# Kernel optimization log

Measured on AMD Instinct MI355X. Metric: run time of the kernel, lower is better.

The kernel has to match this reference:

```python
import jax, jax.numpy as jnp
import numpy as np

B, T, M, P = 512, 64, 256, 256


def setup_inputs() -> dict:
    key = jax.random.key(0)
    ks = jax.random.split(key, 17)
    w = lambda i, shape: (jax.random.normal(ks[i], shape, jnp.float32) * 0.05)
    return {
        "encoded_inputs": jax.random.normal(ks[0], (B, T, M), jnp.float32),
        "y": jax.random.normal(ks[1], (B, T, 1), jnp.float32),
        "tar": jax.random.normal(ks[2], (B, 2), jnp.float32),
        "train": 1,
        "Wd_w": w(3, (M, 2 * P)), "Wd_b": w(4, (M,)),
        "Ud_w": w(5, (M, M)),
        "vd_w": w(6, (1, M)),
        "wt_w": w(7, (1, M + 1)), "wt_b": w(8, (1,)),
        "Wy_w": w(9, (P, P + M)), "Wy_b": w(10, (P,)),
        "vy_w": w(11, (1, P)), "vy_b": w(12, (1,)),
        "Wih": w(13, (4 * P, 1)), "Whh": w(14, (4 * P, P)),
        "bih": w(15, (4 * P,)), "bhh": w(16, (4 * P,)),
    }


def _lstm_cell(x, h, c, Wih, Whh, bih, bhh):
    # torch.nn.LSTMCell gate order: i, f, g, o
    g = x @ Wih.T + h @ Whh.T + (bih + bhh)
    i, f, gg, o = jnp.split(g, 4, axis=1)
    c = jax.nn.sigmoid(f) * c + jax.nn.sigmoid(i) * jnp.tanh(gg)
    h = jax.nn.sigmoid(o) * jnp.tanh(c)
    return h, c


def reference(encoded_inputs, y, tar, train,
              Wd_w, Wd_b, Ud_w, vd_w, wt_w, wt_b,
              Wy_w, Wy_b, vy_w, vy_b, Wih, Whh, bih, bhh):
    Bn = encoded_inputs.shape[0]
    Pn = Whh.shape[1]
    Mn = encoded_inputs.shape[2]
    h0 = jnp.zeros((Bn, Pn), encoded_inputs.dtype)
    c0 = jnp.zeros((Bn, Pn), encoded_inputs.dtype)
    ctx0 = jnp.zeros((Bn, Mn), encoded_inputs.dtype)
    # U_d(encoded_inputs) is loop-invariant
    y1 = jnp.einsum('btm,nm->btn', encoded_inputs, Ud_w)  # (B,T,M)

    def attend(h, s):
        x1 = jnp.concatenate([h, s], axis=1) @ Wd_w.T + Wd_b      # (B,M)
        z1 = jnp.tanh(x1[:, None, :] + y1)                        # (B,T,M)
        l = jnp.einsum('btm,m->bt', z1, vd_w[0])                  # (B,T)
        beta = jax.nn.softmax(l, axis=1)
        return jnp.einsum('bt,btm->bm', beta, encoded_inputs)     # (B,M)

    def step(carry, y_t):
        h, s, _ = carry
        c_t = attend(h, s)
        y_til = jnp.concatenate([c_t, y_t], axis=1) @ wt_w.T + wt_b  # (B,1)
        h, s = _lstm_cell(y_til, h, s, Wih, Whh, bih, bhh)
        return (h, s, c_t), None

    (h, s, c_t), _ = jax.lax.scan(step, (h0, c0, ctx0), jnp.swapaxes(y, 0, 1))

    def head(h):
        return (jnp.concatenate([h, c_t], axis=1) @ Wy_w.T + Wy_b) @ vy_w.T + vy_b

    def extra(h, s, inp):
        y_til = jnp.concatenate([c_t, inp], axis=1) @ wt_w.T + wt_b
        h, s = _lstm_cell(y_til, h, s, Wih, Whh, bih, bhh)
        return h, s, head(h)

    y_Tp1 = head(h)
    if train:
        h, s, y_Tp2 = extra(h, s, tar[:, 0:1])
        h, s, y_Tp3 = extra(h, s, tar[:, 1:2])
    else:
        h, s, y_Tp2 = extra(h, s, y_Tp1)
        h, s, y_Tp3 = extra(h, s, y_Tp2)
    return (y_Tp1, y_Tp2, y_Tp3)
```

## Files before the change

kernel.cpp:

```cpp
#include <hip/hip_runtime.h>


typedef unsigned short u16;
typedef unsigned int u32;
typedef _Float16 half_t;
typedef half_t h2 __attribute__((ext_vector_type(2)));

#define BB 512
#define TT 64
#define MM 256
#define PP 256
#define YS 264

#define WD16_OFF  0
#define WHH16_OFF 131072
#define WY16_OFF  393216
#define WQ_ELEMS  524288
#define E16_OFF   524288
#define E16_ELEMS (BB * TT * MM)
#define WS_ELEMS  (WQ_ELEMS + E16_ELEMS)
#define WS_BYTES  (WS_ELEMS * 2)

struct H8 { h2 p[4]; };

#if defined(__has_builtin)
#if __has_builtin(__builtin_amdgcn_fdot2)
#define FDOT2(a, b, c) __builtin_amdgcn_fdot2((a), (b), (c), false)
#endif
#endif
#ifndef FDOT2
__device__ __forceinline__ float FDOT2(h2 a, h2 b, float c) {
  return c + (float)a[0] * (float)b[0] + (float)a[1] * (float)b[1];
}
#endif

__device__ __forceinline__ float dot8(const H8 w, const H8 a, float acc) {
  acc = FDOT2(w.p[0], a.p[0], acc);
  acc = FDOT2(w.p[1], a.p[1], acc);
  acc = FDOT2(w.p[2], a.p[2], acc);
  acc = FDOT2(w.p[3], a.p[3], acc);
  return acc;
}
__device__ __forceinline__ u16 f2h(float f) {
  union { half_t h; u16 u; } x; x.h = (half_t)f; return x.u;
}
__device__ __forceinline__ void unpackH8(const H8 v, float f[8]) {
#pragma unroll
  for (int i = 0; i < 8; ++i) f[i] = (float)v.p[i >> 1][i & 1];
}
__device__ __forceinline__ void ldf8(const float* p, float f[8]) {
  float4 a = *(const float4*)p;
  float4 b = *(const float4*)(p + 4);
  f[0]=a.x; f[1]=a.y; f[2]=a.z; f[3]=a.w;
  f[4]=b.x; f[5]=b.y; f[6]=b.z; f[7]=b.w;
}
__device__ __forceinline__ float tanh_fast(float x) {
  float e = __builtin_amdgcn_exp2f(x * 2.885390081777927f);
  return 1.0f - 2.0f * __builtin_amdgcn_rcpf(1.0f + e);
}
__device__ __forceinline__ float sigmoid_fast(float x) {
  float e = __builtin_amdgcn_exp2f(x * -1.4426950408889634f);
  return __builtin_amdgcn_rcpf(1.0f + e);
}

__global__ __launch_bounds__(256) void prep_w(
    const float* __restrict__ Wd, const float* __restrict__ Whh,
    const float* __restrict__ Wy, u16* __restrict__ o) {
  int i = blockIdx.x * 256 + threadIdx.x;
  float v;
  if (i < WHH16_OFF) {
    int ki = i & 7, n = (i >> 3) & 255, kb = i >> 11;
    v = Wd[n * 512 + kb * 8 + ki];
  } else if (i < WY16_OFF) {
    int r = i - WHH16_OFF;
    int ki = r & 7, n = (r >> 3) & 1023, kb = r >> 13;
    v = Whh[n * 256 + kb * 8 + ki];
  } else {
    int r = i - WY16_OFF;
    int ki = r & 7, n = (r >> 3) & 255, kb = r >> 11;
    v = Wy[n * 512 + kb * 8 + ki];
  }
  o[i] = f2h(v);
}

__global__ __launch_bounds__(256) void prep_e(
    const float* __restrict__ E, u16* __restrict__ o) {
  int i = blockIdx.x * 256 + threadIdx.x;
  o[E16_OFF + i] = f2h(E[i]);
}

template <int WQ>
__global__ __launch_bounds__(512, 2) void scan_kernel(
    const float* __restrict__ E,
    const float* __restrict__ yin,
    const float* __restrict__ tar,
    const int*   __restrict__ train,
    const void*  __restrict__ Wd_q,
    const float* __restrict__ Wd_b,
    const float* __restrict__ Ud_w,
    const float* __restrict__ vd_w,
    const float* __restrict__ wt_w,
    const float* __restrict__ wt_b,
    const void*  __restrict__ Wy_q,
    const float* __restrict__ Wy_b,
    const float* __restrict__ vy_w,
    const float* __restrict__ vy_b,
    const float* __restrict__ Wih,
    const void*  __restrict__ Whh_q,
    const float* __restrict__ bih,
    const float* __restrict__ bhh,
    const u16*   __restrict__ E16,
    float* __restrict__ out)
{
  __shared__ __align__(16) u16   y1l[2][TT * YS];
  __shared__ __align__(16) u32   hs16[2 * 256];
  __shared__ __align__(16) u32   ctx16p[2 * 128];
  __shared__ __align__(16) float gbuf[2][1024];
  __shared__ __align__(16) float part[2][2][256];
  __shared__ __align__(16) float x1s[2][MM];
  __shared__ __align__(16) float ctx[2][MM];
  __shared__ __align__(16) float lpart[2][4][TT];
  __shared__ float red[2][4];
  __shared__ float sc_head[2];

  const int tid  = threadIdx.x;
  const int half = tid >> 8;
  const int j    = tid & 255;
  const int wv   = (tid >> 6) & 3;
  const int lane = tid & 63;
  const int b    = blockIdx.x * 2 + half;

  hs16[tid] = 0;
  float creg = 0.f;

  {
    const float* __restrict__ Eb = E + (size_t)b * TT * MM;
    const float* __restrict__ Uj = Ud_w + (size_t)j * MM;
    for (int t0 = 0; t0 < TT; t0 += 16) {
      float acc[16];
#pragma unroll
      for (int i = 0; i < 16; ++i) acc[i] = 0.f;
      for (int m0 = 0; m0 < MM; m0 += 8) {
        float w[8]; ldf8(Uj + m0, w);
#pragma unroll
        for (int tt = 0; tt < 16; ++tt) {
          float e[8]; ldf8(Eb + (size_t)(t0 + tt) * MM + m0, e);
#pragma unroll
          for (int mm = 0; mm < 8; ++mm) acc[tt] = fmaf(e[mm], w[mm], acc[tt]);
        }
      }
#pragma unroll
      for (int tt = 0; tt < 16; ++tt)
        y1l[half][(t0 + tt) * YS + j] = f2h(acc[tt]);
    }
  }
  __syncthreads();

  auto whh_mv = [&]() {
    float b00 = 0.f, b01 = 0.f, b10 = 0.f, b11 = 0.f;
    if (WQ) {
      const u16* p1 = (const u16*)Whh_q + (size_t)tid * 8;
      const u16* p2 = p1 + 512 * 8;
#pragma unroll 4
      for (int kb = 0; kb < 32; ++kb) {
        H8 h0 = *(const H8*)&hs16[kb * 4];
        H8 h1 = *(const H8*)&hs16[256 + kb * 4];
        H8 w1 = *(const H8*)p1; p1 += 8192;
        H8 w2 = *(const H8*)p2; p2 += 8192;
        b00 = dot8(w1, h0, b00);
        b01 = dot8(w1, h1, b01);
        b10 = dot8(w2, h0, b10);
        b11 = dot8(w2, h1, b11);
      }
    } else {
      const float* q1 = (const float*)Whh_q + (size_t)tid * 256;
      const float* q2 = q1 + 512 * 256;
#pragma unroll 2
      for (int kb = 0; kb < 32; ++kb) {
        H8 h0 = *(const H8*)&hs16[kb * 4];
        H8 h1 = *(const H8*)&hs16[256 + kb * 4];
        float f0[8], f1[8]; unpackH8(h0, f0); unpackH8(h1, f1);
        float w1[8], w2[8];
        ldf8(q1 + kb * 8, w1);
        ldf8(q2 + kb * 8, w2);
#pragma unroll
        for (int i = 0; i < 8; ++i) {
          b00 = fmaf(f0[i], w1[i], b00);
          b01 = fmaf(f1[i], w1[i], b01);
          b10 = fmaf(f0[i], w2[i], b10);
          b11 = fmaf(f1[i], w2[i], b11);
        }
      }
    }
    gbuf[0][tid] = b00;       gbuf[1][tid] = b01;
    gbuf[0][tid + 512] = b10; gbuf[1][tid + 512] = b11;
  };

  auto gates_apply = [&](float ytil) {
    float g0 = gbuf[half][j]       + ytil * Wih[j]       + bih[j]       + bhh[j];
    float g1 = gbuf[half][j + 256] + ytil * Wih[j + 256] + bih[j + 256] + bhh[j + 256];
    float g2 = gbuf[half][j + 512] + ytil * Wih[j + 512] + bih[j + 512] + bhh[j + 512];
    float g3 = gbuf[half][j + 768] + ytil * Wih[j + 768] + bih[j + 768] + bhh[j + 768];
    float c = sigmoid_fast(g1) * creg + sigmoid_fast(g0) * tanh_fast(g2);
    float h = sigmoid_fast(g3) * tanh_fast(c);
    creg = c;
    u16* hsu = (u16*)hs16;
    hsu[half * 512 + j]       = f2h(h);
    hsu[half * 512 + 256 + j] = f2h(c);
  };

  auto head_store = [&](int outIdx) {
    float p0 = 0.f, p1 = 0.f;
    if (WQ) {
      const u16* pw = (const u16*)Wy_q + (size_t)half * 32 * 2048 + (size_t)j * 8;
      const u32* a0 = half ? &ctx16p[0] : &hs16[0];
      const u32* a1 = half ? &ctx16p[128] : &hs16[256];
#pragma unroll 4
      for (int kb = 0; kb < 32; ++kb) {
        H8 w = *(const H8*)pw; pw += 2048;
        p0 = dot8(w, *(const H8*)&a0[kb * 4], p0);
        p1 = dot8(w, *(const H8*)&a1[kb * 4], p1);
      }
    } else {
      const float* pw = (const float*)Wy_q + (size_t)j * 512 + half * 256;
      for (int kb = 0; kb < 32; ++kb) {
        float w[8]; ldf8(pw + kb * 8, w);
        if (half) {
#pragma unroll
          for (int i = 0; i < 8; ++i) {
            p0 = fmaf(ctx[0][kb * 8 + i], w[i], p0);
            p1 = fmaf(ctx[1][kb * 8 + i], w[i], p1);
          }
        } else {
          H8 h0 = *(const H8*)&hs16[kb * 4];
          H8 h1 = *(const H8*)&hs16[256 + kb * 4];
          float f0[8], f1[8]; unpackH8(h0, f0); unpackH8(h1, f1);
#pragma unroll
          for (int i = 0; i < 8; ++i) {
            p0 = fmaf(f0[i], w[i], p0);
            p1 = fmaf(f1[i], w[i], p1);
          }
        }
      }
    }
    part[half][0][j] = p0;
    part[half][1][j] = p1;
    __syncthreads();
    {
      float hp = part[0][half][j] + part[1][half][j] + Wy_b[j];
      float pp = hp * vy_w[j];
#pragma unroll
      for (int off = 32; off; off >>= 1) pp += __shfl_xor(pp, off, 64);
      if (lane == 0) red[half][wv] = pp;
    }
    __syncthreads();
    if (j == 0) {
      float o = red[half][0] + red[half][1] + red[half][2] + red[half][3]
              + vy_b[0];
      out[(size_t)outIdx * BB + b] = o;
      sc_head[half] = o;
    }
    __syncthreads();
  };

  for (int step = 0; step < TT; ++step) {
    {
      float ax0 = 0.f, ax1 = 0.f;
      float b00 = 0.f, b01 = 0.f, b10 = 0.f, b11 = 0.f;
      if (WQ) {
        const u16* pd = (const u16*)Wd_q + (size_t)half * 32 * 2048 + (size_t)j * 8;
        const u16* p1 = (const u16*)Whh_q + (size_t)tid * 8;
        const u16* p2 = p1 + 512 * 8;
        const int ao = half * 128;
#pragma unroll 4
        for (int kb = 0; kb < 32; ++kb) {
          H8 h0 = *(const H8*)&hs16[kb * 4];
          H8 h1 = *(const H8*)&hs16[256 + kb * 4];
          H8 a0 = *(const H8*)&hs16[ao + kb * 4];
          H8 a1 = *(const H8*)&hs16[256 + ao + kb * 4];
          H8 wd = *(const H8*)pd; pd += 2048;
          H8 w1 = *(const H8*)p1; p1 += 8192;
          H8 w2 = *(const H8*)p2; p2 += 8192;
          ax0 = dot8(wd, a0, ax0);
          ax1 = dot8(wd, a1, ax1);
          b00 = dot8(w1, h0, b00);
          b01 = dot8(w1, h1, b01);
          b10 = dot8(w2, h0, b10);
          b11 = dot8(w2, h1, b11);
        }
      } else {
        const float* pd = (const float*)Wd_q + (size_t)j * 512 + half * 256;
        const float* q1 = (const float*)Whh_q + (size_t)tid * 256;
        const float* q2 = q1 + 512 * 256;
        const int ao = half * 128;
#pragma unroll 2
        for (int kb = 0; kb < 32; ++kb) {
          H8 h0 = *(const H8*)&hs16[kb * 4];
          H8 h1 = *(const H8*)&hs16[256 + kb * 4];
          H8 c0 = *(const H8*)&hs16[ao + kb * 4];
          H8 c1 = *(const H8*)&hs16[256 + ao + kb * 4];
          float f0[8], f1[8], e0[8], e1[8];
          unpackH8(h0, f0); unpackH8(h1, f1); unpackH8(c0, e0); unpackH8(c1, e1);
          float wd[8], w1[8], w2[8];
          ldf8(pd + kb * 8, wd);
          ldf8(q1 + kb * 8, w1);
          ldf8(q2 + kb * 8, w2);
#pragma unroll
          for (int i = 0; i < 8; ++i) {
            ax0 = fmaf(e0[i], wd[i], ax0);
            ax1 = fmaf(e1[i], wd[i], ax1);
            b00 = fmaf(f0[i], w1[i], b00);
            b01 = fmaf(f1[i], w1[i], b01);
            b10 = fmaf(f0[i], w2[i], b10);
            b11 = fmaf(f1[i], w2[i], b11);
          }
        }
      }
      part[half][0][j] = ax0;
      part[half][1][j] = ax1;
      gbuf[0][tid] = b00;       gbuf[1][tid] = b01;
      gbuf[0][tid + 512] = b10; gbuf[1][tid + 512] = b11;
    }
    __syncthreads();
    x1s[half][j] = part[0][half][j] + part[1][half][j] + Wd_b[j];
    __syncthreads();

    {
      const u16* __restrict__ yrow = &y1l[half][lane * YS + wv * 64];
      const float* __restrict__ xp = &x1s[half][wv * 64];
      const float* __restrict__ vp = vd_w + wv * 64;
      float lp = 0.f;
#pragma unroll 2
      for (int m0 = 0; m0 < 64; m0 += 8) {
        H8 yv = *(const H8*)(yrow + m0);
        float yf[8]; unpackH8(yv, yf);
        float xf[8]; ldf8(xp + m0, xf);
        float vf[8]; ldf8(vp + m0, vf);
#pragma unroll
        for (int mm = 0; mm < 8; ++mm) {
          float z = tanh_fast(xf[mm] + yf[mm]);
          lp = fmaf(z, vf[mm], lp);
        }
      }
      lpart[half][wv][lane] = lp;
    }
    __syncthreads();

    float ctv;
    {
      float l = lpart[half][0][lane] + lpart[half][1][lane]
              + lpart[half][2][lane] + lpart[half][3][lane];
      float mx = l;
#pragma unroll
      for (int off = 32; off; off >>= 1) mx = fmaxf(mx, __shfl_xor(mx, off, 64));
      float e = __builtin_amdgcn_exp2f((l - mx) * 1.4426950408889634f);
      float sm = e;
#pragma unroll
      for (int off = 32; off; off >>= 1) sm += __shfl_xor(sm, off, 64);
      float beta = e * __builtin_amdgcn_rcpf(sm);

      float acc = 0.f;
      if (WQ) {
        const half_t* __restrict__ ep = (const half_t*)E16 + (size_t)b * TT * MM + j;
#pragma unroll 8
        for (int t = 0; t < TT; ++t) {
          float bt = __shfl(beta, t, 64);
          acc = fmaf(bt, (float)ep[(size_t)t * MM], acc);
        }
      } else {
        const float* __restrict__ ep = E + (size_t)b * TT * MM + j;
#pragma unroll 8
        for (int t = 0; t < TT; ++t) {
          float bt = __shfl(beta, t, 64);
          acc = fmaf(bt, ep[(size_t)t * MM], acc);
        }
      }
      ctv = acc;
      ctx[half][j] = acc;
      ((u16*)ctx16p)[half * 256 + j] = f2h(acc);

      float p = ctv * wt_w[j];
#pragma unroll
      for (int off = 32; off; off >>= 1) p += __shfl_xor(p, off, 64);
      if (lane == 0) red[half][wv] = p;
    }
    __syncthreads();

    {
      float ytil = red[half][0] + red[half][1] + red[half][2] + red[half][3]
                 + yin[(size_t)b * TT + step] * wt_w[MM] + wt_b[0];
      gates_apply(ytil);
    }
    __syncthreads();
  }

  float ctdot;
  {
    float p = ctx[half][j] * wt_w[j];
#pragma unroll
    for (int off = 32; off; off >>= 1) p += __shfl_xor(p, off, 64);
    if (lane == 0) red[half][wv] = p;
    __syncthreads();
    ctdot = red[half][0] + red[half][1] + red[half][2] + red[half][3];
  }

  head_store(0);

  const int tr = train[0];
  for (int e = 0; e < 2; ++e) {
    float inp = tr ? tar[(size_t)b * 2 + e] : sc_head[half];
    float ytil = ctdot + inp * wt_w[MM] + wt_b[0];
    whh_mv();
    __syncthreads();
    gates_apply(ytil);
    __syncthreads();
    head_store(1 + e);
  }
}

extern "C" void kernel_launch(void* const* d_in, const int* in_sizes, int n_in,
                              void* d_out, int out_size, void* d_ws, size_t ws_size,
                              hipStream_t stream) {
  const float* E     = (const float*)d_in[0];
  const float* yin   = (const float*)d_in[1];
  const float* tar   = (const float*)d_in[2];
  const int*   train = (const int*)d_in[3];
  const float* Wd_w  = (const float*)d_in[4];
  const float* Wd_b  = (const float*)d_in[5];
  const float* Ud_w  = (const float*)d_in[6];
  const float* vd_w  = (const float*)d_in[7];
  const float* wt_w  = (const float*)d_in[8];
  const float* wt_b  = (const float*)d_in[9];
  const float* Wy_w  = (const float*)d_in[10];
  const float* Wy_b  = (const float*)d_in[11];
  const float* vy_w  = (const float*)d_in[12];
  const float* vy_b  = (const float*)d_in[13];
  const float* Wih   = (const float*)d_in[14];
  const float* Whh   = (const float*)d_in[15];
  const float* bih   = (const float*)d_in[16];
  const float* bhh   = (const float*)d_in[17];

  float* out = (float*)d_out;

  if (ws_size >= (size_t)WS_BYTES) {
    u16* wq = (u16*)d_ws;
    prep_w<<<dim3(WQ_ELEMS / 256), dim3(256), 0, stream>>>(Wd_w, Whh, Wy_w, wq);
    prep_e<<<dim3(E16_ELEMS / 256), dim3(256), 0, stream>>>(E, wq);
    scan_kernel<1><<<dim3(BB / 2), dim3(512), 0, stream>>>(
        E, yin, tar, train, wq + WD16_OFF, Wd_b, Ud_w, vd_w, wt_w, wt_b,
        wq + WY16_OFF, Wy_b, vy_w, vy_b, Wih, wq + WHH16_OFF, bih, bhh,
        wq + E16_OFF, out);
  } else {
    scan_kernel<0><<<dim3(BB / 2), dim3(512), 0, stream>>>(
        E, yin, tar, train, Wd_w, Wd_b, Ud_w, vd_w, wt_w, wt_b,
        Wy_w, Wy_b, vy_w, vy_b, Wih, Whh, bih, bhh, (const u16*)nullptr, out);
  }

  (void)in_sizes; (void)n_in; (void)out_size;
}
```

Measured before the change: 1.195 ms.

## Double block to 1024 threads, split matvecs along K, and use fp16 Ud projection

The scan kernel now runs 1024 threads per block, still covering two batch rows. The Wd, Wy and context reductions are split across four or two K-partitions with shared-memory partial sums, and each Whh gate row gets its own thread. The Ud_w projection is precomputed into an fp16 packed layout and computed with fdot2 from the fp16 E copy. This exposes more parallelism per recurrent step in exchange for extra barriers and partial-sum traffic, and possibly lower occupancy because of the 1024-thread launch bound and register pressure.

```diff
diff --git a/kernel.cpp b/kernel.cpp
--- a/kernel.cpp
+++ b/kernel.cpp
@@ -15,11 +15,12 @@
 #define WD16_OFF  0
 #define WHH16_OFF 131072
 #define WY16_OFF  393216
-#define WQ_ELEMS  524288
-#define E16_OFF   524288
+#define UD16_OFF  524288
+#define WPREP_ELEMS 589824
+#define E16_OFF   589824
 #define E16_ELEMS (BB * TT * MM)
-#define WS_ELEMS  (WQ_ELEMS + E16_ELEMS)
-#define WS_BYTES  (WS_ELEMS * 2)
+#define WS_ELEMS  (WPREP_ELEMS + E16_ELEMS)
+#define WS_BYTES  ((size_t)WS_ELEMS * 2)
 
 struct H8 { h2 p[4]; };
 
@@ -65,7 +66,8 @@
 
 __global__ __launch_bounds__(256) void prep_w(
     const float* __restrict__ Wd, const float* __restrict__ Whh,
-    const float* __restrict__ Wy, u16* __restrict__ o) {
+    const float* __restrict__ Wy, const float* __restrict__ Ud,
+    u16* __restrict__ o) {
   int i = blockIdx.x * 256 + threadIdx.x;
   float v;
   if (i < WHH16_OFF) {
@@ -75,10 +77,14 @@
     int r = i - WHH16_OFF;
     int ki = r & 7, n = (r >> 3) & 1023, kb = r >> 13;
     v = Whh[n * 256 + kb * 8 + ki];
-  } else {
+  } else if (i < UD16_OFF) {
     int r = i - WY16_OFF;
     int ki = r & 7, n = (r >> 3) & 255, kb = r >> 11;
     v = Wy[n * 512 + kb * 8 + ki];
+  } else {
+    int r = i - UD16_OFF;
+    int ki = r & 7, n = (r >> 3) & 255, kb = r >> 11;
+    v = Ud[n * 256 + kb * 8 + ki];
   }
   o[i] = f2h(v);
 }
@@ -90,14 +96,14 @@
 }
 
 template <int WQ>
-__global__ __launch_bounds__(512, 2) void scan_kernel(
+__global__ __launch_bounds__(1024, 4) void scan_kernel(
     const float* __restrict__ E,
     const float* __restrict__ yin,
     const float* __restrict__ tar,
     const int*   __restrict__ train,
     const void*  __restrict__ Wd_q,
     const float* __restrict__ Wd_b,
-    const float* __restrict__ Ud_w,
+    const void*  __restrict__ Ud_q,
     const float* __restrict__ vd_w,
     const float* __restrict__ wt_w,
     const float* __restrict__ wt_b,
@@ -113,152 +119,157 @@
     float* __restrict__ out)
 {
   __shared__ __align__(16) u16   y1l[2][TT * YS];
-  __shared__ __align__(16) u32   hs16[2 * 256];
-  __shared__ __align__(16) u32   ctx16p[2 * 128];
+  __shared__ __align__(16) u32   hs16[2][256];
+  __shared__ __align__(16) u32   ctx16p[2][128];
+  __shared__ __align__(16) float ctx[2][256];
+  __shared__ __align__(16) float x1s[2][256];
+  __shared__ __align__(16) float part[4][2][256];
+  __shared__ __align__(16) float part2[2][2][256];
   __shared__ __align__(16) float gbuf[2][1024];
-  __shared__ __align__(16) float part[2][2][256];
-  __shared__ __align__(16) float x1s[2][MM];
-  __shared__ __align__(16) float ctx[2][MM];
-  __shared__ __align__(16) float lpart[2][4][TT];
-  __shared__ float red[2][4];
+  __shared__ __align__(16) float lpart[2][8][64];
+  __shared__ float red[2][4], red2[2][4];
   __shared__ float sc_head[2];
 
   const int tid  = threadIdx.x;
-  const int half = tid >> 8;
-  const int j    = tid & 255;
-  const int wv   = (tid >> 6) & 3;
   const int lane = tid & 63;
-  const int b    = blockIdx.x * 2 + half;
-
-  hs16[tid] = 0;
+  const int w    = tid >> 6;
+  const int n    = tid & 255;
+  const int kq   = tid >> 8;
+  const int rw   = w >> 2;
+  const int jj   = (w & 3) * 64 + lane;
+  const int r1   = w >> 3;
+  const int mq   = w & 7;
+  const int kh   = (w >> 2) & 1;
+  const int j2   = (w & 3) * 64 + lane;
+
+  if (tid < 512) ((u32*)hs16)[tid] = 0;
   float creg = 0.f;
 
   {
-    const float* __restrict__ Eb = E + (size_t)b * TT * MM;
-    const float* __restrict__ Uj = Ud_w + (size_t)j * MM;
-    for (int t0 = 0; t0 < TT; t0 += 16) {
-      float acc[16];
-#pragma unroll
-      for (int i = 0; i < 16; ++i) acc[i] = 0.f;
-      for (int m0 = 0; m0 < MM; m0 += 8) {
-        float w[8]; ldf8(Uj + m0, w);
-#pragma unroll
-        for (int tt = 0; tt < 16; ++tt) {
-          float e[8]; ldf8(Eb + (size_t)(t0 + tt) * MM + m0, e);
-#pragma unroll
-          for (int mm = 0; mm < 8; ++mm) acc[tt] = fmaf(e[mm], w[mm], acc[tt]);
-        }
-      }
-#pragma unroll
-      for (int tt = 0; tt < 16; ++tt)
-        y1l[half][(t0 + tt) * YS + j] = f2h(acc[tt]);
+    const int yr  = kq >> 1;
+    const int th  = kq & 1;
+    const int bb  = blockIdx.x * 2 + yr;
+    if (WQ) {
+      const half_t* __restrict__ Ef = (const half_t*)E16;
+      for (int t = th * 32; t < th * 32 + 32; ++t) {
+        const half_t* ee = Ef + ((size_t)bb * TT + t) * MM;
+        const u16* pu = (const u16*)Ud_q + (size_t)n * 8;
+        float acc = 0.f;
+#pragma unroll 8
+        for (int kb = 0; kb < 32; ++kb) {
+          H8 uw = *(const H8*)pu; pu += 2048;
+          H8 ev = *(const H8*)(ee + kb * 8);
+          acc = dot8(uw, ev, acc);
+        }
+        y1l[yr][t * YS + n] = f2h(acc);
+      }
+    } else {
+      const float* __restrict__ Eb = E + (size_t)bb * TT * MM;
+      const float* __restrict__ Uj = (const float*)Ud_q + (size_t)n * MM;
+      for (int t = th * 32; t < th * 32 + 32; ++t) {
+        float acc = 0.f;
+        for (int m0 = 0; m0 < MM; m0 += 8) {
+          float uu[8], ee[8];
+          ldf8(Uj + m0, uu);
+          ldf8(Eb + (size_t)t * MM + m0, ee);
+#pragma unroll
+          for (int i = 0; i < 8; ++i) acc = fmaf(uu[i], ee[i], acc);
+        }
+        y1l[yr][t * YS + n] = f2h(acc);
+      }
     }
   }
   __syncthreads();
 
   auto whh_mv = [&]() {
-    float b00 = 0.f, b01 = 0.f, b10 = 0.f, b11 = 0.f;
+    float b0 = 0.f, b1 = 0.f;
     if (WQ) {
-      const u16* p1 = (const u16*)Whh_q + (size_t)tid * 8;
-      const u16* p2 = p1 + 512 * 8;
+      const u16* ph = (const u16*)Whh_q + (size_t)tid * 8;
+#pragma unroll 8
+      for (int kb = 0; kb < 32; ++kb) {
+        H8 w8 = *(const H8*)ph; ph += 8192;
+        b0 = dot8(w8, *(const H8*)&hs16[0][kb * 4], b0);
+        b1 = dot8(w8, *(const H8*)&hs16[1][kb * 4], b1);
+      }
+    } else {
+      const float* ph = (const float*)Whh_q + (size_t)tid * 256;
 #pragma unroll 4
       for (int kb = 0; kb < 32; ++kb) {
-        H8 h0 = *(const H8*)&hs16[kb * 4];
-        H8 h1 = *(const H8*)&hs16[256 + kb * 4];
-        H8 w1 = *(const H8*)p1; p1 += 8192;
-        H8 w2 = *(const H8*)p2; p2 += 8192;
-        b00 = dot8(w1, h0, b00);
-        b01 = dot8(w1, h1, b01);
-        b10 = dot8(w2, h0, b10);
-        b11 = dot8(w2, h1, b11);
-      }
-    } else {
-      const float* q1 = (const float*)Whh_q + (size_t)tid * 256;
-      const float* q2 = q1 + 512 * 256;
-#pragma unroll 2
-      for (int kb = 0; kb < 32; ++kb) {
-        H8 h0 = *(const H8*)&hs16[kb * 4];
-        H8 h1 = *(const H8*)&hs16[256 + kb * 4];
-        float f0[8], f1[8]; unpackH8(h0, f0); unpackH8(h1, f1);
-        float w1[8], w2[8];
-        ldf8(q1 + kb * 8, w1);
-        ldf8(q2 + kb * 8, w2);
+        float w8[8]; ldf8(ph + kb * 8, w8);
+        float f0[8], f1[8];
+        unpackH8(*(const H8*)&hs16[0][kb * 4], f0);
+        unpackH8(*(const H8*)&hs16[1][kb * 4], f1);
 #pragma unroll
         for (int i = 0; i < 8; ++i) {
-          b00 = fmaf(f0[i], w1[i], b00);
-          b01 = fmaf(f1[i], w1[i], b01);
-          b10 = fmaf(f0[i], w2[i], b10);
-          b11 = fmaf(f1[i], w2[i], b11);
-        }
-      }
-    }
-    gbuf[0][tid] = b00;       gbuf[1][tid] = b01;
-    gbuf[0][tid + 512] = b10; gbuf[1][tid + 512] = b11;
+          b0 = fmaf(f0[i], w8[i], b0);
+          b1 = fmaf(f1[i], w8[i], b1);
+        }
+      }
+    }
+    gbuf[0][tid] = b0;
+    gbuf[1][tid] = b1;
   };
 
   auto gates_apply = [&](float ytil) {
-    float g0 = gbuf[half][j]       + ytil * Wih[j]       + bih[j]       + bhh[j];
-    float g1 = gbuf[half][j + 256] + ytil * Wih[j + 256] + bih[j + 256] + bhh[j + 256];
-    float g2 = gbuf[half][j + 512] + ytil * Wih[j + 512] + bih[j + 512] + bhh[j + 512];
-    float g3 = gbuf[half][j + 768] + ytil * Wih[j + 768] + bih[j + 768] + bhh[j + 768];
+    float g0 = gbuf[rw][jj]       + ytil * Wih[jj]       + bih[jj]       + bhh[jj];
+    float g1 = gbuf[rw][jj + 256] + ytil * Wih[jj + 256] + bih[jj + 256] + bhh[jj + 256];
+    float g2 = gbuf[rw][jj + 512] + ytil * Wih[jj + 512] + bih[jj + 512] + bhh[jj + 512];
+    float g3 = gbuf[rw][jj + 768] + ytil * Wih[jj + 768] + bih[jj + 768] + bhh[jj + 768];
     float c = sigmoid_fast(g1) * creg + sigmoid_fast(g0) * tanh_fast(g2);
     float h = sigmoid_fast(g3) * tanh_fast(c);
     creg = c;
-    u16* hsu = (u16*)hs16;
-    hsu[half * 512 + j]       = f2h(h);
-    hsu[half * 512 + 256 + j] = f2h(c);
+    ((u16*)&hs16[rw][0])[jj]       = f2h(h);
+    ((u16*)&hs16[rw][0])[256 + jj] = f2h(c);
   };
 
   auto head_store = [&](int outIdx) {
     float p0 = 0.f, p1 = 0.f;
     if (WQ) {
-      const u16* pw = (const u16*)Wy_q + (size_t)half * 32 * 2048 + (size_t)j * 8;
-      const u32* a0 = half ? &ctx16p[0] : &hs16[0];
-      const u32* a1 = half ? &ctx16p[128] : &hs16[256];
-#pragma unroll 4
-      for (int kb = 0; kb < 32; ++kb) {
-        H8 w = *(const H8*)pw; pw += 2048;
-        p0 = dot8(w, *(const H8*)&a0[kb * 4], p0);
-        p1 = dot8(w, *(const H8*)&a1[kb * 4], p1);
+      const u16* pw = (const u16*)Wy_q + ((size_t)(kq * 16) * 256 + n) * 8;
+      const u32* a0 = (kq < 2) ? &hs16[0][kq * 64] : &ctx16p[0][(kq - 2) * 64];
+      const u32* a1 = (kq < 2) ? &hs16[1][kq * 64] : &ctx16p[1][(kq - 2) * 64];
+#pragma unroll 8
+      for (int i = 0; i < 16; ++i) {
+        H8 w8 = *(const H8*)pw; pw += 2048;
+        p0 = dot8(w8, *(const H8*)&a0[i * 4], p0);
+        p1 = dot8(w8, *(const H8*)&a1[i * 4], p1);
       }
     } else {
-      const float* pw = (const float*)Wy_q + (size_t)j * 512 + half * 256;
-      for (int kb = 0; kb < 32; ++kb) {
-        float w[8]; ldf8(pw + kb * 8, w);
-        if (half) {
-#pragma unroll
-          for (int i = 0; i < 8; ++i) {
-            p0 = fmaf(ctx[0][kb * 8 + i], w[i], p0);
-            p1 = fmaf(ctx[1][kb * 8 + i], w[i], p1);
-          }
+      const float* pw = (const float*)Wy_q + (size_t)n * 512 + kq * 128;
+      for (int i = 0; i < 16; ++i) {
+        float w8[8]; ldf8(pw + i * 8, w8);
+        int kb = kq * 16 + i;
+        float f0[8], f1[8];
+        if (kb < 32) {
+          unpackH8(*(const H8*)&hs16[0][kb * 4], f0);
+          unpackH8(*(const H8*)&hs16[1][kb * 4], f1);
         } else {
-          H8 h0 = *(const H8*)&hs16[kb * 4];
-          H8 h1 = *(const H8*)&hs16[256 + kb * 4];
-          float f0[8], f1[8]; unpackH8(h0, f0); unpackH8(h1, f1);
-#pragma unroll
-          for (int i = 0; i < 8; ++i) {
-            p0 = fmaf(f0[i], w[i], p0);
-            p1 = fmaf(f1[i], w[i], p1);
-          }
-        }
-      }
-    }
-    part[half][0][j] = p0;
-    part[half][1][j] = p1;
-    __syncthreads();
-    {
-      float hp = part[0][half][j] + part[1][half][j] + Wy_b[j];
-      float pp = hp * vy_w[j];
+          ldf8(&ctx[0][(kb - 32) * 8], f0);
+          ldf8(&ctx[1][(kb - 32) * 8], f1);
+        }
+#pragma unroll
+        for (int i2 = 0; i2 < 8; ++i2) {
+          p0 = fmaf(f0[i2], w8[i2], p0);
+          p1 = fmaf(f1[i2], w8[i2], p1);
+        }
+      }
+    }
+    part[kq][0][n] = p0;
+    part[kq][1][n] = p1;
+    __syncthreads();
+    if (w < 8) {
+      float hp = part[0][rw][jj] + part[1][rw][jj] + part[2][rw][jj]
+               + part[3][rw][jj] + Wy_b[jj];
+      float pp = hp * vy_w[jj];
 #pragma unroll
       for (int off = 32; off; off >>= 1) pp += __shfl_xor(pp, off, 64);
-      if (lane == 0) red[half][wv] = pp;
-    }
-    __syncthreads();
-    if (j == 0) {
-      float o = red[half][0] + red[half][1] + red[half][2] + red[half][3]
-              + vy_b[0];
-      out[(size_t)outIdx * BB + b] = o;
-      sc_head[half] = o;
+      if (lane == 0) red[rw][w & 3] = pp;
+    }
+    __syncthreads();
+    if (w < 8 && (w & 3) == 0 && lane == 0) {
+      float o = red[rw][0] + red[rw][1] + red[rw][2] + red[rw][3] + vy_b[0];
+      out[(size_t)outIdx * BB + blockIdx.x * 2 + rw] = o;
+      sc_head[rw] = o;
     }
     __syncthreads();
   };
@@ -266,72 +277,51 @@
   for (int step = 0; step < TT; ++step) {
     {
       float ax0 = 0.f, ax1 = 0.f;
-      float b00 = 0.f, b01 = 0.f, b10 = 0.f, b11 = 0.f;
       if (WQ) {
-        const u16* pd = (const u16*)Wd_q + (size_t)half * 32 * 2048 + (size_t)j * 8;
-        const u16* p1 = (const u16*)Whh_q + (size_t)tid * 8;
-        const u16* p2 = p1 + 512 * 8;
-        const int ao = half * 128;
-#pragma unroll 4
-        for (int kb = 0; kb < 32; ++kb) {
-          H8 h0 = *(const H8*)&hs16[kb * 4];
-          H8 h1 = *(const H8*)&hs16[256 + kb * 4];
-          H8 a0 = *(const H8*)&hs16[ao + kb * 4];
-          H8 a1 = *(const H8*)&hs16[256 + ao + kb * 4];
-          H8 wd = *(const H8*)pd; pd += 2048;
-          H8 w1 = *(const H8*)p1; p1 += 8192;
-          H8 w2 = *(const H8*)p2; p2 += 8192;
-          ax0 = dot8(wd, a0, ax0);
-          ax1 = dot8(wd, a1, ax1);
-          b00 = dot8(w1, h0, b00);
-          b01 = dot8(w1, h1, b01);
-          b10 = dot8(w2, h0, b10);
-          b11 = dot8(w2, h1, b11);
+        const u16* pd = (const u16*)Wd_q + ((size_t)(kq * 16) * 256 + n) * 8;
+        const u32* a0 = (kq < 2) ? &hs16[0][kq * 64] : &hs16[0][128 + (kq - 2) * 64];
+        const u32* a1 = (kq < 2) ? &hs16[1][kq * 64] : &hs16[1][128 + (kq - 2) * 64];
+#pragma unroll 8
+        for (int i = 0; i < 16; ++i) {
+          H8 w8 = *(const H8*)pd; pd += 2048;
+          ax0 = dot8(w8, *(const H8*)&a0[i * 4], ax0);
+          ax1 = dot8(w8, *(const H8*)&a1[i * 4], ax1);
         }
       } else {
-        const float* pd = (const float*)Wd_q + (size_t)j * 512 + half * 256;
-        const float* q1 = (const float*)Whh_q + (size_t)tid * 256;
-        const float* q2 = q1 + 512 * 256;
-        const int ao = half * 128;
-#pragma unroll 2
-        for (int kb = 0; kb < 32; ++kb) {
-          H8 h0 = *(const H8*)&hs16[kb * 4];
-          H8 h1 = *(const H8*)&hs16[256 + kb * 4];
-          H8 c0 = *(const H8*)&hs16[ao + kb * 4];
-          H8 c1 = *(const H8*)&hs16[256 + ao + kb * 4];
-          float f0[8], f1[8], e0[8], e1[8];
-          unpackH8(h0, f0); unpackH8(h1, f1); unpackH8(c0, e0); unpackH8(c1, e1);
-          float wd[8], w1[8], w2[8];
-          ldf8(pd + kb * 8, wd);
-          ldf8(q1 + kb * 8, w1);
-          ldf8(q2 + kb * 8, w2);
-#pragma unroll
-          for (int i = 0; i < 8; ++i) {
-            ax0 = fmaf(e0[i], wd[i], ax0);
-            ax1 = fmaf(e1[i], wd[i], ax1);
-            b00 = fmaf(f0[i], w1[i], b00);
-            b01 = fmaf(f1[i], w1[i], b01);
-            b10 = fmaf(f0[i], w2[i], b10);
-            b11 = fmaf(f1[i], w2[i], b11);
+        const float* pd = (const float*)Wd_q + (size_t)n * 512 + kq * 128;
+        const u32* a0 = (kq < 2) ? &hs16[0][kq * 64] : &hs16[0][128 + (kq - 2) * 64];
+        const u32* a1 = (kq < 2) ? &hs16[1][kq * 64] : &hs16[1][128 + (kq - 2) * 64];
+        for (int i = 0; i < 16; ++i) {
+          float w8[8]; ldf8(pd + i * 8, w8);
+          float f0[8], f1[8];
+          unpackH8(*(const H8*)&a0[i * 4], f0);
+          unpackH8(*(const H8*)&a1[i * 4], f1);
+#pragma unroll
+          for (int i2 = 0; i2 < 8; ++i2) {
+            ax0 = fmaf(f0[i2], w8[i2], ax0);
+            ax1 = fmaf(f1[i2], w8[i2], ax1);
           }
         }
       }
-      part[half][0][j] = ax0;
-      part[half][1][j] = ax1;
-      gbuf[0][tid] = b00;       gbuf[1][tid] = b01;
-      gbuf[0][tid + 512] = b10; gbuf[1][tid + 512] = b11;
-    }
-    __syncthreads();
-    x1s[half][j] = part[0][half][j] + part[1][half][j] + Wd_b[j];
+      part[kq][0][n] = ax0;
+      part[kq][1][n] = ax1;
+      whh_mv();
+    }
+    __syncthreads();
+
+    if (w < 8) {
+      x1s[rw][jj] = part[0][rw][jj] + part[1][rw][jj] + part[2][rw][jj]
+                  + part[3][rw][jj] + Wd_b[jj];
+    }
     __syncthreads();
 
     {
-      const u16* __restrict__ yrow = &y1l[half][lane * YS + wv * 64];
-      const float* __restrict__ xp = &x1s[half][wv * 64];
-      const float* __restrict__ vp = vd_w + wv * 64;
+      const u16* __restrict__ yrow = &y1l[r1][lane * YS + mq * 32];
+      const float* __restrict__ xp = &x1s[r1][mq * 32];
+      const float* __restrict__ vp = vd_w + mq * 32;
       float lp = 0.f;
-#pragma unroll 2
-      for (int m0 = 0; m0 < 64; m0 += 8) {
+#pragma unroll
+      for (int m0 = 0; m0 < 32; m0 += 8) {
         H8 yv = *(const H8*)(yrow + m0);
         float yf[8]; unpackH8(yv, yf);
         float xf[8]; ldf8(xp + m0, xf);
@@ -342,14 +332,14 @@
           lp = fmaf(z, vf[mm], lp);
         }
       }
-      lpart[half][wv][lane] = lp;
-    }
-    __syncthreads();
-
-    float ctv;
+      lpart[r1][mq][lane] = lp;
+    }
+    __syncthreads();
+
     {
-      float l = lpart[half][0][lane] + lpart[half][1][lane]
-              + lpart[half][2][lane] + lpart[half][3][lane];
+      float l = 0.f;
+#pragma unroll
+      for (int q = 0; q < 8; ++q) l += lpart[r1][q][lane];
       float mx = l;
 #pragma unroll
       for (int off = 32; off; off >>= 1) mx = fmaxf(mx, __shfl_xor(mx, off, 64));
@@ -359,60 +349,70 @@
       for (int off = 32; off; off >>= 1) sm += __shfl_xor(sm, off, 64);
       float beta = e * __builtin_amdgcn_rcpf(sm);
 
+      const int bb = blockIdx.x * 2 + r1;
       float acc = 0.f;
       if (WQ) {
-        const half_t* __restrict__ ep = (const half_t*)E16 + (size_t)b * TT * MM + j;
-#pragma unroll 8
-        for (int t = 0; t < TT; ++t) {
-          float bt = __shfl(beta, t, 64);
-          acc = fmaf(bt, (float)ep[(size_t)t * MM], acc);
+        const half_t* __restrict__ ep =
+            (const half_t*)E16 + ((size_t)bb * TT + kh * 32) * MM + j2;
+#pragma unroll 8
+        for (int i = 0; i < 32; ++i) {
+          float bt = __shfl(beta, kh * 32 + i, 64);
+          acc = fmaf(bt, (float)ep[(size_t)i * MM], acc);
         }
       } else {
-        const float* __restrict__ ep = E + (size_t)b * TT * MM + j;
-#pragma unroll 8
-        for (int t = 0; t < TT; ++t) {
-          float bt = __shfl(beta, t, 64);
-          acc = fmaf(bt, ep[(size_t)t * MM], acc);
-        }
-      }
-      ctv = acc;
-      ctx[half][j] = acc;
-      ((u16*)ctx16p)[half * 256 + j] = f2h(acc);
-
-      float p = ctv * wt_w[j];
+        const float* __restrict__ ep =
+            E + ((size_t)bb * TT + kh * 32) * MM + j2;
+#pragma unroll 8
+        for (int i = 0; i < 32; ++i) {
+          float bt = __shfl(beta, kh * 32 + i, 64);
+          acc = fmaf(bt, ep[(size_t)i * MM], acc);
+        }
+      }
+      part2[r1][kh][j2] = acc;
+    }
+    __syncthreads();
+
+    if (w < 8) {
+      float ct = part2[rw][0][jj] + part2[rw][1][jj];
+      ctx[rw][jj] = ct;
+      ((u16*)&ctx16p[rw][0])[jj] = f2h(ct);
+      float p = ct * wt_w[jj];
 #pragma unroll
       for (int off = 32; off; off >>= 1) p += __shfl_xor(p, off, 64);
-      if (lane == 0) red[half][wv] = p;
-    }
-    __syncthreads();
-
-    {
-      float ytil = red[half][0] + red[half][1] + red[half][2] + red[half][3]
-                 + yin[(size_t)b * TT + step] * wt_w[MM] + wt_b[0];
+      if (lane == 0) red[rw][w & 3] = p;
+    }
+    __syncthreads();
+
+    if (w < 8) {
+      const int bb = blockIdx.x * 2 + rw;
+      float ytil = red[rw][0] + red[rw][1] + red[rw][2] + red[rw][3]
+                 + yin[(size_t)bb * TT + step] * wt_w[MM] + wt_b[0];
       gates_apply(ytil);
     }
     __syncthreads();
   }
 
-  float ctdot;
-  {
-    float p = ctx[half][j] * wt_w[j];
+  if (w < 8) {
+    float p = ctx[rw][jj] * wt_w[jj];
 #pragma unroll
     for (int off = 32; off; off >>= 1) p += __shfl_xor(p, off, 64);
-    if (lane == 0) red[half][wv] = p;
-    __syncthreads();
-    ctdot = red[half][0] + red[half][1] + red[half][2] + red[half][3];
-  }
+    if (lane == 0) red2[rw][w & 3] = p;
+  }
+  __syncthreads();
 
   head_store(0);
 
   const int tr = train[0];
   for (int e = 0; e < 2; ++e) {
-    float inp = tr ? tar[(size_t)b * 2 + e] : sc_head[half];
-    float ytil = ctdot + inp * wt_w[MM] + wt_b[0];
     whh_mv();
     __syncthreads();
-    gates_apply(ytil);
+    if (w < 8) {
+      const int bb = blockIdx.x * 2 + rw;
+      float inp = tr ? tar[(size_t)bb * 2 + e] : sc_head[rw];
+      float ytil = red2[rw][0] + red2[rw][1] + red2[rw][2] + red2[rw][3]
+                 + inp * wt_w[MM] + wt_b[0];
+      gates_apply(ytil);
+    }
     __syncthreads();
     head_store(1 + e);
   }
@@ -442,16 +442,17 @@
 
   float* out = (float*)d_out;
 
-  if (ws_size >= (size_t)WS_BYTES) {
+  if (ws_size >= WS_BYTES) {
     u16* wq = (u16*)d_ws;
-    prep_w<<<dim3(WQ_ELEMS / 256), dim3(256), 0, stream>>>(Wd_w, Whh, Wy_w, wq);
+    prep_w<<<dim3(WPREP_ELEMS / 256), dim3(256), 0, stream>>>(
+        Wd_w, Whh, Wy_w, Ud_w, wq);
     prep_e<<<dim3(E16_ELEMS / 256), dim3(256), 0, stream>>>(E, wq);
-    scan_kernel<1><<<dim3(BB / 2), dim3(512), 0, stream>>>(
-        E, yin, tar, train, wq + WD16_OFF, Wd_b, Ud_w, vd_w, wt_w, wt_b,
-        wq + WY16_OFF, Wy_b, vy_w, vy_b, Wih, wq + WHH16_OFF, bih, bhh,
+    scan_kernel<1><<<dim3(BB / 2), dim3(1024), 0, stream>>>(
+        E, yin, tar, train, wq + WD16_OFF, Wd_b, wq + UD16_OFF, vd_w, wt_w,
+        wt_b, wq + WY16_OFF, Wy_b, vy_w, vy_b, Wih, wq + WHH16_OFF, bih, bhh,
         wq + E16_OFF, out);
   } else {
-    scan_kernel<0><<<dim3(BB / 2), dim3(512), 0, stream>>>(
+    scan_kernel<0><<<dim3(BB / 2), dim3(1024), 0, stream>>>(
         E, yin, tar, train, Wd_w, Wd_b, Ud_w, vd_w, wt_w, wt_b,
         Wy_w, Wy_b, vy_w, vy_b, Wih, Whh, bih, bhh, (const u16*)nullptr, out);
   }
```

New measurement: 1.503 ms. 25.8% more time.
